# Optimization experiments

Hardware: AMD Instinct MI355X
Metric: run time of the kernel (lower is better)

## Reference

```python
import jax, jax.numpy as jnp
import numpy as np

NUM_STAGES = 8
NUM_CODES = 1024  # 2**10
DATA_DIM = 256
N = 131072
EPS = 1e-12


def setup_inputs() -> dict:
    key = jax.random.key(0)
    k1, k2, k3 = jax.random.split(key, 3)
    input_data = jax.random.normal(k1, (N, DATA_DIM), dtype=jnp.float32)
    # Uniform(-1/K, 1/K) init as in torch __init__
    codebooks = jax.random.uniform(k2, (NUM_STAGES, NUM_CODES, DATA_DIM), dtype=jnp.float32,
                                   minval=-1.0 / NUM_CODES, maxval=1.0 / NUM_CODES)
    noise = jax.random.normal(k3, (N, DATA_DIM), dtype=jnp.float32)
    codebooks_used = jnp.zeros((NUM_STAGES, NUM_CODES), dtype=jnp.int32)
    return {"input_data": input_data, "codebooks": codebooks, "noise": noise,
            "codebooks_used": codebooks_used, "train_mode": 1}


def _hard_vq(residual, cb):
    # expanded-norm pairwise squared distances: [N, K]
    d = (jnp.sum(residual * residual, axis=1, keepdims=True)
         - 2.0 * residual @ cb.T
         + jnp.sum(cb * cb, axis=1)[None, :])
    idx = jnp.argmin(d, axis=1)            # [N]
    q = cb[idx]                            # gather [N, D]
    return q, residual - q, idx


def reference(input_data, codebooks, noise, codebooks_used, train_mode):
    residual = input_data
    total_q = jnp.zeros_like(input_data)
    used = codebooks_used
    for i in range(NUM_STAGES):  # static, sequential residual dependency
        q, residual, idx = _hard_vq(residual, codebooks[i])
        total_q = total_q + q
        # torch `a[idx] += 1` with duplicate indices increments each touched
        # code only ONCE; replicate via presence mask.
        presence = jnp.zeros((NUM_CODES,), dtype=jnp.int32).at[idx].set(1)
        used = used.at[i].add(presence)
    if train_mode:
        err_norm = jnp.sqrt(jnp.sum((input_data - total_q) ** 2, axis=1, keepdims=True))
        noise_norm = jnp.sqrt(jnp.sum(noise * noise, axis=1, keepdims=True))
        out = input_data + (err_norm / noise_norm + EPS) * noise
    else:
        out = total_q
    return out, used
```

## Files before the change

### kernel.cpp

```cpp
#include <hip/hip_runtime.h>
#include <math.h>

#define NSTAGES 8
#define NCODES  1024
#define DIM     256
#define NROWS   131072
#define TM      64
#define EPSV    1e-12f

typedef __attribute__((ext_vector_type(8))) short bf16x8;
typedef __attribute__((ext_vector_type(4))) float f32x4;

__device__ __forceinline__ unsigned fkey(float f) {
    unsigned u = __float_as_uint(f);
    return (u & 0x80000000u) ? ~u : (u | 0x80000000u);
}
__device__ __forceinline__ short f2bf(float f) {
    unsigned u = __float_as_uint(f);
    u = u + 0x7fffu + ((u >> 16) & 1u);
    return (short)(u >> 16);
}
__device__ __forceinline__ float bf2f(short h) {
    return __uint_as_float(((unsigned)(unsigned short)h) << 16);
}

__global__ __launch_bounds__(256) void prep_kernel(const float* __restrict__ cb,
                                                   short* __restrict__ chF,
                                                   short* __restrict__ clF,
                                                   float* __restrict__ cn) {
    __shared__ float tile[64][260];
    __shared__ float pr[256];
    int s  = blockIdx.x >> 4;
    int c0 = (blockIdx.x & 15) * 64;
    int t  = threadIdx.x;
    const float4* src = (const float4*)(cb + ((size_t)s * NCODES + c0) * DIM);
#pragma unroll
    for (int i = 0; i < 16; ++i) {
        int e4 = t + 256 * i;
        int c  = e4 >> 6;
        int d4 = (e4 & 63) * 4;
        *(float4*)&tile[c][d4] = src[e4];
    }
    __syncthreads();
    {
        int c = t >> 2, q = t & 3;
        float sum = 0.f;
#pragma unroll 16
        for (int d = q * 64; d < q * 64 + 64; ++d) { float x = tile[c][d]; sum += x * x; }
        pr[t] = sum;
    }
    __syncthreads();
    if (t < 64) cn[(size_t)s * NCODES + c0 + t] = pr[4*t] + pr[4*t+1] + pr[4*t+2] + pr[4*t+3];
#pragma unroll
    for (int i = 0; i < 8; ++i) {
        int fi   = t + 256 * i;
        int nt_l = fi >> 9;
        int rem  = fi & 511;
        int ks   = rem >> 6;
        int lf   = rem & 63;
        int q    = lf >> 4;
        int nl   = lf & 15;
        int code = nt_l * 16 + nl;
        int kb   = ks * 32 + q * 8;
        bf16x8 hh, ll;
#pragma unroll
        for (int j = 0; j < 8; ++j) {
            float v = tile[code][kb + j];
            short h = f2bf(v);
            hh[j] = h;
            ll[j] = f2bf(v - bf2f(h));
        }
        size_t off = ((((size_t)s * 64 + (c0 >> 4) + nt_l) * 8 + ks) * 64 + lf) * 8;
        *(bf16x8*)&chF[off] = hh;
        *(bf16x8*)&clF[off] = ll;
    }
}

__global__ void init_used_kernel(const int* __restrict__ cbu, float* __restrict__ used) {
    int i = blockIdx.x * 256 + threadIdx.x;
    if (i < NSTAGES * NCODES) used[i] = (float)cbu[i];
}

__global__ __launch_bounds__(256, 2) void rvq_kernel(const float* __restrict__ input,
                                                     const float* __restrict__ cb,
                                                     const short* __restrict__ chF,
                                                     const short* __restrict__ clF,
                                                     const float* __restrict__ cn,
                                                     const float* __restrict__ noise,
                                                     const int* __restrict__ cbu,
                                                     const int* __restrict__ tmp,
                                                     float* __restrict__ out,
                                                     float* __restrict__ used) {
    __shared__ __align__(16) short rhF[4 * 8 * 64 * 8];
    __shared__ __align__(16) short rlF[4 * 8 * 64 * 8];
    __shared__ unsigned long long bestkey[TM];
    __shared__ float pr[256], pn[256], scl[TM];

    int t    = threadIdx.x;
    int w    = t >> 6;
    int lane = t & 63;
    int row0 = blockIdx.x * TM;
    int row  = t >> 2;
    int q4   = t & 3;
    const float* inp = input + (size_t)row0 * DIM;

    {
        const float4* ip4 = (const float4*)(inp + row * DIM + q4 * 64);
#pragma unroll
        for (int a = 0; a < 2; ++a) {
            int ks = q4 * 2 + a;
#pragma unroll
            for (int b = 0; b < 4; ++b) {
                float4 v0 = ip4[a * 8 + b * 2];
                float4 v1 = ip4[a * 8 + b * 2 + 1];
                float v[8] = {v0.x, v0.y, v0.z, v0.w, v1.x, v1.y, v1.z, v1.w};
                bf16x8 hh, ll;
#pragma unroll
                for (int j = 0; j < 8; ++j) {
                    short h = f2bf(v[j]);
                    hh[j] = h;
                    ll[j] = f2bf(v[j] - bf2f(h));
                }
                int off = (((row >> 4) * 8 + ks) * 64 + b * 16 + (row & 15)) * 8;
                *(bf16x8*)&rhF[off] = hh;
                *(bf16x8*)&rlF[off] = ll;
            }
        }
    }
    if (t < TM) bestkey[t] = ~0ULL;

#pragma unroll 1
    for (int s = 0; s < NSTAGES; ++s) {
        __syncthreads();

        const short* chW = chF + ((((size_t)s * 64 + w * 16) * 8) * 64 + lane) * 8;
        const short* clW = clF + ((((size_t)s * 64 + w * 16) * 8) * 64 + lane) * 8;
        const float* cnL = cn + (size_t)s * NCODES + w * 256 + (lane & 15);

        float best[16];
        int   bcode[16];
#pragma unroll
        for (int i = 0; i < 16; ++i) { best[i] = INFINITY; bcode[i] = 0; }

#pragma unroll 1
        for (int cc = 0; cc < 4; ++cc) {
            const short* chC = chW + (size_t)cc * 16384;
            const short* clC = clW + (size_t)cc * 16384;
            float cnn[4];
#pragma unroll
            for (int nn = 0; nn < 4; ++nn) cnn[nn] = cnL[cc * 64 + nn * 16];

            f32x4 acc[4][4];
#pragma unroll
            for (int mt = 0; mt < 4; ++mt)
#pragma unroll
                for (int nn = 0; nn < 4; ++nn) acc[mt][nn] = (f32x4){0.f, 0.f, 0.f, 0.f};

            bf16x8 Bh[2][4], Bl[2][4];
#pragma unroll
            for (int nn = 0; nn < 4; ++nn) {
                Bh[0][nn] = *(const bf16x8*)&chC[nn * 4096];
                Bl[0][nn] = *(const bf16x8*)&clC[nn * 4096];
            }
#pragma unroll 2
            for (int ks = 0; ks < 8; ++ks) {
                int cur = ks & 1;
                int nxt = cur ^ 1;
                if (ks < 7) {
#pragma unroll
                    for (int nn = 0; nn < 4; ++nn) {
                        Bh[nxt][nn] = *(const bf16x8*)&chC[nn * 4096 + (ks + 1) * 512];
                        Bl[nxt][nn] = *(const bf16x8*)&clC[nn * 4096 + (ks + 1) * 512];
                    }
                }
                bf16x8 Ah[4], Al[4];
#pragma unroll
                for (int mt = 0; mt < 4; ++mt) {
                    int offA = ((mt * 8 + ks) * 64 + lane) * 8;
                    Ah[mt] = *(const bf16x8*)&rhF[offA];
                    Al[mt] = *(const bf16x8*)&rlF[offA];
                }
#pragma unroll
                for (int mt = 0; mt < 4; ++mt)
#pragma unroll
                    for (int nn = 0; nn < 4; ++nn) {
                        acc[mt][nn] = __builtin_amdgcn_mfma_f32_16x16x32_bf16(Al[mt], Bh[cur][nn], acc[mt][nn], 0, 0, 0);
                        acc[mt][nn] = __builtin_amdgcn_mfma_f32_16x16x32_bf16(Ah[mt], Bl[cur][nn], acc[mt][nn], 0, 0, 0);
                        acc[mt][nn] = __builtin_amdgcn_mfma_f32_16x16x32_bf16(Ah[mt], Bh[cur][nn], acc[mt][nn], 0, 0, 0);
                    }
            }
            int code0 = w * 256 + cc * 64 + (lane & 15);
#pragma unroll
            for (int mt = 0; mt < 4; ++mt)
#pragma unroll
                for (int nn = 0; nn < 4; ++nn) {
                    int code = code0 + nn * 16;
                    float cno = cnn[nn];
#pragma unroll
                    for (int r = 0; r < 4; ++r) {
                        float sc = cno - 2.0f * acc[mt][nn][r];
                        int mi = mt * 4 + r;
                        if (sc < best[mi]) { best[mi] = sc; bcode[mi] = code; }
                    }
                }
        }
        unsigned long long mk[16];
#pragma unroll
        for (int i = 0; i < 16; ++i)
            mk[i] = ((unsigned long long)fkey(best[i]) << 32) | (unsigned)bcode[i];
#pragma unroll
        for (int d = 1; d < 16; d <<= 1)
#pragma unroll
            for (int i = 0; i < 16; ++i) {
                unsigned long long o = __shfl_xor(mk[i], d);
                if (o < mk[i]) mk[i] = o;
            }
        if ((lane & 15) == 0) {
#pragma unroll
            for (int mt = 0; mt < 4; ++mt)
#pragma unroll
                for (int r = 0; r < 4; ++r)
                    atomicMin(&bestkey[mt * 16 + (lane >> 4) * 4 + r], mk[mt * 4 + r]);
        }
        __syncthreads();

        {
            int idx = (int)(bestkey[row] & 0xffffffffu);
            const float4* cp = (const float4*)(cb + ((size_t)s * NCODES + idx) * DIM + q4 * 64);
#pragma unroll
            for (int a = 0; a < 2; ++a) {
                int ks = q4 * 2 + a;
#pragma unroll
                for (int b = 0; b < 4; ++b) {
                    int off = (((row >> 4) * 8 + ks) * 64 + b * 16 + (row & 15)) * 8;
                    bf16x8 hh = *(bf16x8*)&rhF[off];
                    bf16x8 ll = *(bf16x8*)&rlF[off];
                    float4 c0 = cp[a * 8 + b * 2];
                    float4 c1 = cp[a * 8 + b * 2 + 1];
                    float cv[8] = {c0.x, c0.y, c0.z, c0.w, c1.x, c1.y, c1.z, c1.w};
#pragma unroll
                    for (int j = 0; j < 8; ++j) {
                        float v = bf2f(hh[j]) + bf2f(ll[j]) - cv[j];
                        short h = f2bf(v);
                        hh[j] = h;
                        ll[j] = f2bf(v - bf2f(h));
                    }
                    *(bf16x8*)&rhF[off] = hh;
                    *(bf16x8*)&rlF[off] = ll;
                }
            }
            if (t < TM) {
                int gi = (s << 10) + (int)(bestkey[t] & 0xffffffffu);
                used[gi] = (float)cbu[gi] + 1.0f;
            }
        }
        __syncthreads();
        if (t < TM) bestkey[t] = ~0ULL;
    }

    float sr = 0.f, sn = 0.f;
    {
        const float4* np4 = (const float4*)(noise + (size_t)(row0 + row) * DIM + q4 * 64);
#pragma unroll
        for (int a = 0; a < 2; ++a) {
            int ks = q4 * 2 + a;
#pragma unroll
            for (int b = 0; b < 4; ++b) {
                int off = (((row >> 4) * 8 + ks) * 64 + b * 16 + (row & 15)) * 8;
                bf16x8 hh = *(bf16x8*)&rhF[off];
                bf16x8 ll = *(bf16x8*)&rlF[off];
#pragma unroll
                for (int j = 0; j < 8; ++j) {
                    float v = bf2f(hh[j]) + bf2f(ll[j]);
                    sr += v * v;
                }
            }
        }
#pragma unroll
        for (int i = 0; i < 16; ++i) {
            float4 nv = np4[i];
            sn += nv.x*nv.x + nv.y*nv.y + nv.z*nv.z + nv.w*nv.w;
        }
    }
    pr[t] = sr; pn[t] = sn;
    __syncthreads();
    if (t < TM) {
        float rs = pr[4*t] + pr[4*t+1] + pr[4*t+2] + pr[4*t+3];
        float ns = pn[4*t] + pn[4*t+1] + pn[4*t+2] + pn[4*t+3];
        scl[t] = sqrtf(rs) / sqrtf(ns) + EPSV;
    }
    __syncthreads();
    int tm = tmp[0];
    if (tm) {
        const float4* ib = (const float4*)inp;
        const float4* nb = (const float4*)(noise + (size_t)row0 * DIM);
        float4* ob = (float4*)(out + (size_t)row0 * DIM);
#pragma unroll
        for (int i = 0; i < 16; ++i) {
            int e4 = t + 256 * i;
            int r  = e4 >> 6;
            float sc = scl[r];
            float4 iv = ib[e4];
            float4 nv = nb[e4];
            float4 ov;
            ov.x = iv.x + sc * nv.x; ov.y = iv.y + sc * nv.y;
            ov.z = iv.z + sc * nv.z; ov.w = iv.w + sc * nv.w;
            ob[e4] = ov;
        }
    } else {
        float* op = out + (size_t)(row0 + row) * DIM + q4 * 64;
        const float* ipq = inp + row * DIM + q4 * 64;
#pragma unroll
        for (int a = 0; a < 2; ++a) {
            int ks = q4 * 2 + a;
#pragma unroll
            for (int b = 0; b < 4; ++b) {
                int off = (((row >> 4) * 8 + ks) * 64 + b * 16 + (row & 15)) * 8;
                bf16x8 hh = *(bf16x8*)&rhF[off];
                bf16x8 ll = *(bf16x8*)&rlF[off];
#pragma unroll
                for (int j = 0; j < 8; ++j) {
                    int d = a * 32 + b * 8 + j;
                    op[d] = ipq[d] - (bf2f(hh[j]) + bf2f(ll[j]));
                }
            }
        }
    }
}

extern "C" void kernel_launch(void* const* d_in, const int* in_sizes, int n_in,
                              void* d_out, int out_size, void* d_ws, size_t ws_size,
                              hipStream_t stream) {
    const float* input = (const float*)d_in[0];
    const float* cb    = (const float*)d_in[1];
    const float* noise = (const float*)d_in[2];
    const int*   cbu   = (const int*)d_in[3];
    const int*   tm    = (const int*)d_in[4];
    float* out  = (float*)d_out;
    float* used = out + (size_t)NROWS * DIM;

    short* chF = (short*)d_ws;
    short* clF = chF + (size_t)NSTAGES * 64 * 8 * 64 * 8;
    float* cn  = (float*)(clF + (size_t)NSTAGES * 64 * 8 * 64 * 8);

    prep_kernel<<<NSTAGES * 16, 256, 0, stream>>>(cb, chF, clF, cn);
    init_used_kernel<<<(NSTAGES * NCODES + 255) / 256, 256, 0, stream>>>(cbu, used);
    rvq_kernel<<<NROWS / TM, 256, 0, stream>>>(input, cb, chF, clF, cn, noise, cbu, tm, out, used);
}
```

Baseline: 1.579 ms.

## Deepen codebook prefetch across chunks and stages, pad LDS stride, raise MFMA priority

Codebook B-fragment loads are restructured into a persistent register pipeline. High parts are prefetched two k-steps ahead and low parts one step ahead, and prefetching continues across chunk and stage boundaries so each chunk starts with data already in registers. The LDS residual buffers get a padded k-stride of 520 shorts, meant to reduce bank conflicts. MFMA blocks are wrapped with s_setprio, and the bf16 hi/lo split reuses the rounded high value instead of converting it back. The deeper pipeline and full unroll raise register pressure under launch bounds of 2 blocks per CU, which risks spills.

```diff
diff --git a/kernel.cpp b/kernel.cpp
--- a/kernel.cpp
+++ b/kernel.cpp
@@ -8,6 +8,8 @@
 #define TM      64
 #define EPSV    1e-12f
 
+#define KSTRIDE 520
+
 typedef __attribute__((ext_vector_type(8))) short bf16x8;
 typedef __attribute__((ext_vector_type(4))) float f32x4;
 
@@ -15,13 +17,15 @@
     unsigned u = __float_as_uint(f);
     return (u & 0x80000000u) ? ~u : (u | 0x80000000u);
 }
-__device__ __forceinline__ short f2bf(float f) {
-    unsigned u = __float_as_uint(f);
-    u = u + 0x7fffu + ((u >> 16) & 1u);
-    return (short)(u >> 16);
-}
 __device__ __forceinline__ float bf2f(short h) {
     return __uint_as_float(((unsigned)(unsigned short)h) << 16);
+}
+__device__ __forceinline__ void split2(float v, short& h, short& l) {
+    unsigned u  = __float_as_uint(v);
+    unsigned hr = u + 0x7fffu + ((u >> 16) & 1u);
+    h = (short)(hr >> 16);
+    float hf = __uint_as_float(hr & 0xffff0000u);
+    l = (short)(__float_as_uint(v - hf) >> 16);
 }
 
 __global__ __launch_bounds__(256) void prep_kernel(const float* __restrict__ cb,
@@ -65,10 +69,10 @@
         bf16x8 hh, ll;
 #pragma unroll
         for (int j = 0; j < 8; ++j) {
-            float v = tile[code][kb + j];
-            short h = f2bf(v);
+            short h, l;
+            split2(tile[code][kb + j], h, l);
             hh[j] = h;
-            ll[j] = f2bf(v - bf2f(h));
+            ll[j] = l;
         }
         size_t off = ((((size_t)s * 64 + (c0 >> 4) + nt_l) * 8 + ks) * 64 + lf) * 8;
         *(bf16x8*)&chF[off] = hh;
@@ -91,8 +95,8 @@
                                                      const int* __restrict__ tmp,
                                                      float* __restrict__ out,
                                                      float* __restrict__ used) {
-    __shared__ __align__(16) short rhF[4 * 8 * 64 * 8];
-    __shared__ __align__(16) short rlF[4 * 8 * 64 * 8];
+    __shared__ __align__(16) short rhF[4 * 8 * KSTRIDE];
+    __shared__ __align__(16) short rlF[4 * 8 * KSTRIDE];
     __shared__ unsigned long long bestkey[TM];
     __shared__ float pr[256], pn[256], scl[TM];
 
@@ -117,17 +121,30 @@
                 bf16x8 hh, ll;
 #pragma unroll
                 for (int j = 0; j < 8; ++j) {
-                    short h = f2bf(v[j]);
+                    short h, l;
+                    split2(v[j], h, l);
                     hh[j] = h;
-                    ll[j] = f2bf(v[j] - bf2f(h));
-                }
-                int off = (((row >> 4) * 8 + ks) * 64 + b * 16 + (row & 15)) * 8;
+                    ll[j] = l;
+                }
+                int off = ((row >> 4) * 8 + ks) * KSTRIDE + (b * 16 + (row & 15)) * 8;
                 *(bf16x8*)&rhF[off] = hh;
                 *(bf16x8*)&rlF[off] = ll;
             }
         }
     }
     if (t < TM) bestkey[t] = ~0ULL;
+
+    bf16x8 Bh[4][4], Bl[2][4];
+    {
+        const short* chW0 = chF + (((size_t)w * 16) * 8 * 64 + lane) * 8;
+        const short* clW0 = clF + (((size_t)w * 16) * 8 * 64 + lane) * 8;
+#pragma unroll
+        for (int nn = 0; nn < 4; ++nn) {
+            Bh[0][nn] = *(const bf16x8*)&chW0[nn * 4096];
+            Bh[1][nn] = *(const bf16x8*)&chW0[nn * 4096 + 512];
+            Bl[0][nn] = *(const bf16x8*)&clW0[nn * 4096];
+        }
+    }
 
 #pragma unroll 1
     for (int s = 0; s < NSTAGES; ++s) {
@@ -146,6 +163,12 @@
         for (int cc = 0; cc < 4; ++cc) {
             const short* chC = chW + (size_t)cc * 16384;
             const short* clC = clW + (size_t)cc * 16384;
+            const short* chN;
+            const short* clN;
+            bool pfok;
+            if (cc < 3) { chN = chC + 16384; clN = clC + 16384; pfok = true; }
+            else        { chN = chW + 262144; clN = clW + 262144; pfok = (s < 7); }
+
             float cnn[4];
 #pragma unroll
             for (int nn = 0; nn < 4; ++nn) cnn[nn] = cnL[cc * 64 + nn * 16];
@@ -156,38 +179,43 @@
 #pragma unroll
                 for (int nn = 0; nn < 4; ++nn) acc[mt][nn] = (f32x4){0.f, 0.f, 0.f, 0.f};
 
-            bf16x8 Bh[2][4], Bl[2][4];
-#pragma unroll
-            for (int nn = 0; nn < 4; ++nn) {
-                Bh[0][nn] = *(const bf16x8*)&chC[nn * 4096];
-                Bl[0][nn] = *(const bf16x8*)&clC[nn * 4096];
-            }
-#pragma unroll 2
+#pragma unroll
             for (int ks = 0; ks < 8; ++ks) {
-                int cur = ks & 1;
-                int nxt = cur ^ 1;
-                if (ks < 7) {
-#pragma unroll
-                    for (int nn = 0; nn < 4; ++nn) {
-                        Bh[nxt][nn] = *(const bf16x8*)&chC[nn * 4096 + (ks + 1) * 512];
-                        Bl[nxt][nn] = *(const bf16x8*)&clC[nn * 4096 + (ks + 1) * 512];
-                    }
+                if (ks <= 5) {
+#pragma unroll
+                    for (int nn = 0; nn < 4; ++nn)
+                        Bh[(ks + 2) & 3][nn] = *(const bf16x8*)&chC[nn * 4096 + (ks + 2) * 512];
+                } else if (pfok) {
+#pragma unroll
+                    for (int nn = 0; nn < 4; ++nn)
+                        Bh[(ks + 2) & 3][nn] = *(const bf16x8*)&chN[nn * 4096 + (ks - 6) * 512];
+                }
+                if (ks <= 6) {
+#pragma unroll
+                    for (int nn = 0; nn < 4; ++nn)
+                        Bl[(ks + 1) & 1][nn] = *(const bf16x8*)&clC[nn * 4096 + (ks + 1) * 512];
+                } else if (pfok) {
+#pragma unroll
+                    for (int nn = 0; nn < 4; ++nn)
+                        Bl[0][nn] = *(const bf16x8*)&clN[nn * 4096];
                 }
                 bf16x8 Ah[4], Al[4];
 #pragma unroll
                 for (int mt = 0; mt < 4; ++mt) {
-                    int offA = ((mt * 8 + ks) * 64 + lane) * 8;
+                    int offA = (mt * 8 + ks) * KSTRIDE + lane * 8;
                     Ah[mt] = *(const bf16x8*)&rhF[offA];
                     Al[mt] = *(const bf16x8*)&rlF[offA];
                 }
+                __builtin_amdgcn_s_setprio(1);
 #pragma unroll
                 for (int mt = 0; mt < 4; ++mt)
 #pragma unroll
                     for (int nn = 0; nn < 4; ++nn) {
-                        acc[mt][nn] = __builtin_amdgcn_mfma_f32_16x16x32_bf16(Al[mt], Bh[cur][nn], acc[mt][nn], 0, 0, 0);
-                        acc[mt][nn] = __builtin_amdgcn_mfma_f32_16x16x32_bf16(Ah[mt], Bl[cur][nn], acc[mt][nn], 0, 0, 0);
-                        acc[mt][nn] = __builtin_amdgcn_mfma_f32_16x16x32_bf16(Ah[mt], Bh[cur][nn], acc[mt][nn], 0, 0, 0);
+                        acc[mt][nn] = __builtin_amdgcn_mfma_f32_16x16x32_bf16(Al[mt], Bh[ks & 3][nn], acc[mt][nn], 0, 0, 0);
+                        acc[mt][nn] = __builtin_amdgcn_mfma_f32_16x16x32_bf16(Ah[mt], Bl[ks & 1][nn], acc[mt][nn], 0, 0, 0);
+                        acc[mt][nn] = __builtin_amdgcn_mfma_f32_16x16x32_bf16(Ah[mt], Bh[ks & 3][nn], acc[mt][nn], 0, 0, 0);
                     }
+                __builtin_amdgcn_s_setprio(0);
             }
             int code0 = w * 256 + cc * 64 + (lane & 15);
 #pragma unroll
@@ -232,7 +260,7 @@
                 int ks = q4 * 2 + a;
 #pragma unroll
                 for (int b = 0; b < 4; ++b) {
-                    int off = (((row >> 4) * 8 + ks) * 64 + b * 16 + (row & 15)) * 8;
+                    int off = ((row >> 4) * 8 + ks) * KSTRIDE + (b * 16 + (row & 15)) * 8;
                     bf16x8 hh = *(bf16x8*)&rhF[off];
                     bf16x8 ll = *(bf16x8*)&rlF[off];
                     float4 c0 = cp[a * 8 + b * 2];
@@ -241,9 +269,10 @@
 #pragma unroll
                     for (int j = 0; j < 8; ++j) {
                         float v = bf2f(hh[j]) + bf2f(ll[j]) - cv[j];
-                        short h = f2bf(v);
+                        short h, l;
+                        split2(v, h, l);
                         hh[j] = h;
-                        ll[j] = f2bf(v - bf2f(h));
+                        ll[j] = l;
                     }
                     *(bf16x8*)&rhF[off] = hh;
                     *(bf16x8*)&rlF[off] = ll;
@@ -266,7 +295,7 @@
             int ks = q4 * 2 + a;
 #pragma unroll
             for (int b = 0; b < 4; ++b) {
-                int off = (((row >> 4) * 8 + ks) * 64 + b * 16 + (row & 15)) * 8;
+                int off = ((row >> 4) * 8 + ks) * KSTRIDE + (b * 16 + (row & 15)) * 8;
                 bf16x8 hh = *(bf16x8*)&rhF[off];
                 bf16x8 ll = *(bf16x8*)&rlF[off];
 #pragma unroll
@@ -315,7 +344,7 @@
             int ks = q4 * 2 + a;
 #pragma unroll
             for (int b = 0; b < 4; ++b) {
-                int off = (((row >> 4) * 8 + ks) * 64 + b * 16 + (row & 15)) * 8;
+                int off = ((row >> 4) * 8 + ks) * KSTRIDE + (b * 16 + (row & 15)) * 8;
                 bf16x8 hh = *(bf16x8*)&rhF[off];
                 bf16x8 ll = *(bf16x8*)&rlF[off];
 #pragma unroll
```

Measured after the change: 5.609 ms. +255.2%, slower.
